# Performance work log

Measured on AMD Instinct MI355X. Metric: run time of the kernel, lower is better.

## Reference

```python
import jax, jax.numpy as jnp
import numpy as np

B, T, D, H = 2, 2048, 1024, 16
STD = 0.02

def setup_inputs() -> dict:
    key = jax.random.key(0)
    ks = jax.random.split(key, 5)
    x = jax.random.normal(ks[0], (B, T, D), dtype=jnp.float32)
    Wq = jax.random.normal(ks[1], (D, D), dtype=jnp.float32) * STD
    Wk = jax.random.normal(ks[2], (D, D), dtype=jnp.float32) * STD
    Wv = jax.random.normal(ks[3], (D, D), dtype=jnp.float32) * STD
    Wo = jax.random.normal(ks[4], (D, D), dtype=jnp.float32) * STD
    z = jnp.zeros((D,), dtype=jnp.float32)
    return {"x": x, "Wq": Wq, "bq": z, "Wk": Wk, "bk": z, "Wv": Wv, "bv": z, "Wo": Wo, "bo": z}

def _split(t, h):
    b, s, dm = t.shape
    return t.reshape(b, s, h, dm // h).transpose(0, 2, 1, 3)  # (B,h,T,d)

def reference(x, Wq, bq, Wk, bk, Wv, bv, Wo, bo):
    h = H
    # linear projections (nn.Linear: y = x @ W^T + b)
    q = _split(x @ Wq.T + bq, h)
    k = _split(x @ Wk.T + bk, h)
    v = _split(x @ Wv.T + bv, h)
    d_k = k.shape[-1]
    # scaled dot-product similarities (B,h,T,T)
    sim = jnp.einsum("bhqd,bhkd->bhqk", q, k) / jnp.sqrt(jnp.float32(d_k))
    # causal mask: upper triangle (excluding diag) filled with -inf
    Tq = sim.shape[-1]
    causal = jnp.tril(jnp.ones((Tq, Tq), dtype=bool))
    sim = jnp.where(causal, sim, -jnp.inf)
    attn = jax.nn.softmax(sim, axis=-1)
    ctx = jnp.einsum("bhqk,bhkd->bhqd", attn, v)  # (B,h,T,d)
    ctx = ctx.transpose(0, 2, 1, 3).reshape(x.shape[0], x.shape[1], -1)  # (B,T,D)
    return ctx @ Wo.T + bo
```

## Files before the change

kernel.cpp:

```cpp
#include <hip/hip_runtime.h>
#include <hip/hip_bf16.h>


typedef __attribute__((ext_vector_type(8))) short bf16x8;
typedef __attribute__((ext_vector_type(4))) float f32x4;
typedef __attribute__((ext_vector_type(4))) short s16x4;

#define QSCALE 0.18033688011f

__device__ __forceinline__ int sniff_f32(const void* p) {
    const unsigned short* u = (const unsigned short*)p;
    int c = 0;
    for (int i = 0; i < 256; ++i) {
        int e = (u[i] >> 7) & 0xFF;
        c += (e >= 0x90) ? 1 : 0;
    }
    return c > 8;
}

__device__ __forceinline__ void async_copy16(const void* g, void* l) {
    __builtin_amdgcn_global_load_lds(
        (const __attribute__((address_space(1))) void*)g,
        (__attribute__((address_space(3))) void*)l, 16, 0, 0);
}

struct Cvt { const void* src; __hip_bfloat16* dst; int n; };
struct CvtPack { Cvt a[9]; };

__global__ __launch_bounds__(256) void cvt_bf16(CvtPack pk) {
    const Cvt c = pk.a[blockIdx.y];
    const int f32 = sniff_f32(c.src);
    const int stride = gridDim.x * 256 * 8;
    for (int idx = (blockIdx.x * 256 + threadIdx.x) * 8; idx < c.n; idx += stride) {
        if (f32) {
            const float* s = (const float*)c.src + idx;
            f32x4 a0 = *(const f32x4*)s;
            f32x4 a1 = *(const f32x4*)(s + 4);
            union { __hip_bfloat16 h[8]; bf16x8 v; } u;
#pragma unroll
            for (int e = 0; e < 4; e++) u.h[e]     = (__hip_bfloat16)a0[e];
#pragma unroll
            for (int e = 0; e < 4; e++) u.h[4 + e] = (__hip_bfloat16)a1[e];
            *(bf16x8*)&c.dst[idx] = u.v;
        } else {
            *(bf16x8*)&c.dst[idx] = *(const bf16x8*)((const __hip_bfloat16*)c.src + idx);
        }
    }
}

template <int MODE>
__device__ __forceinline__ void gemm_async_body(
    const __hip_bfloat16* __restrict__ A, const __hip_bfloat16* __restrict__ W,
    const __hip_bfloat16* __restrict__ bias, void* __restrict__ C,
    int M, int N, int K, int bm, int bn, float outscale,
    __hip_bfloat16* sA, __hip_bfloat16* sB)
{
    const int tid  = threadIdx.x;
    const int wave = tid >> 6;
    const int lane = tid & 63;
    const int quad = lane >> 4;
    const int l15  = lane & 15;
    const int wr   = wave >> 1;
    const int wc   = wave & 1;

    const int srow = wave * 16 + (lane >> 2);
    const int scol = (lane & 3) * 8;
    const __hip_bfloat16* gA0 = A + (size_t)(bm + srow) * K + scol;
    const __hip_bfloat16* gB0 = W + (size_t)(bn + srow) * K + scol;
    __hip_bfloat16* sA0 = sA + wave * 512;
    __hip_bfloat16* sB0 = sB + wave * 512;

    f32x4 acc[4][4];
#pragma unroll
    for (int i = 0; i < 4; i++)
#pragma unroll
        for (int j = 0; j < 4; j++) acc[i][j] = (f32x4)0.0f;

    for (int k0 = 0; k0 < K; k0 += 32) {
        __syncthreads();
#pragma unroll
        for (int r = 0; r < 2; r++) {
            async_copy16(gA0 + (size_t)r * 64 * K + k0, sA0 + r * 2048);
            async_copy16(gB0 + (size_t)r * 64 * K + k0, sB0 + r * 2048);
        }
        __syncthreads();

        bf16x8 af[4], bf[4];
#pragma unroll
        for (int i = 0; i < 4; i++)
            af[i] = *(const bf16x8*)&sA[(wr * 64 + i * 16 + l15) * 32 + quad * 8];
#pragma unroll
        for (int j = 0; j < 4; j++)
            bf[j] = *(const bf16x8*)&sB[(wc * 64 + j * 16 + l15) * 32 + quad * 8];
#pragma unroll
        for (int i = 0; i < 4; i++)
#pragma unroll
            for (int j = 0; j < 4; j++)
                acc[i][j] = __builtin_amdgcn_mfma_f32_16x16x32_bf16(af[i], bf[j], acc[i][j], 0, 0, 0);
    }

    float bv[4];
#pragma unroll
    for (int j = 0; j < 4; j++)
        bv[j] = (float)bias[bn + wc * 64 + j * 16 + l15];

    if (MODE == 2) {
        __hip_bfloat16* sOut = sA;
        __syncthreads();
#pragma unroll
        for (int i = 0; i < 4; i++) {
            int tl = wr * 64 + i * 16 + quad * 4;
#pragma unroll
            for (int j = 0; j < 4; j++) {
                int dl = wc * 64 + j * 16 + l15;
                union { __hip_bfloat16 e[4]; s16x4 v; } u;
#pragma unroll
                for (int r = 0; r < 4; r++)
                    u.e[r] = (__hip_bfloat16)(acc[i][j][r] + bv[j]);
                *(s16x4*)&sOut[dl * 136 + tl] = u.v;
            }
        }
        __syncthreads();
        __hip_bfloat16* VTo = (__hip_bfloat16*)C;
        const int bb = bm >> 11, tt0 = bm & 2047;
#pragma unroll
        for (int g8 = 0; g8 < 8; g8++) {
            int idx = g8 * 256 + tid;
            int dl  = idx >> 4;
            int tc  = (idx & 15) * 8;
            int dg  = bn + dl;
            bf16x8 v = *(const bf16x8*)&sOut[dl * 136 + tc];
            *(bf16x8*)&VTo[(((size_t)bb * 16 + (dg >> 6)) * 64 + (dg & 63)) * 2048 + tt0 + tc] = v;
        }
    } else {
#pragma unroll
        for (int i = 0; i < 4; i++) {
#pragma unroll
            for (int j = 0; j < 4; j++) {
                int col = bn + wc * 64 + j * 16 + l15;
#pragma unroll
                for (int r = 0; r < 4; r++) {
                    int row = bm + wr * 64 + i * 16 + quad * 4 + r;
                    float v = (acc[i][j][r] + bv[j]) * outscale;
                    if (MODE == 1) ((float*)C)[(size_t)row * N + col] = v;
                    else ((__hip_bfloat16*)C)[(size_t)row * N + col] = (__hip_bfloat16)v;
                }
            }
        }
    }
}

__global__ __launch_bounds__(256, 2) void qkv_gemm(
    const __hip_bfloat16* __restrict__ x,
    const __hip_bfloat16* __restrict__ Wq, const __hip_bfloat16* __restrict__ bq, __hip_bfloat16* __restrict__ Q,
    const __hip_bfloat16* __restrict__ Wk, const __hip_bfloat16* __restrict__ bk, __hip_bfloat16* __restrict__ Kb,
    const __hip_bfloat16* __restrict__ Wv, const __hip_bfloat16* __restrict__ bv, __hip_bfloat16* __restrict__ VT,
    int M, int N, int K)
{
    __shared__ __hip_bfloat16 smem[128 * 136];
    __hip_bfloat16* sA = smem;
    __hip_bfloat16* sB = smem + 128 * 32;
    if (blockIdx.z == 0)
        gemm_async_body<0>(x, Wq, bq, Q, M, N, K, blockIdx.x * 128, blockIdx.y * 128, QSCALE, sA, sB);
    else if (blockIdx.z == 1)
        gemm_async_body<0>(x, Wk, bk, Kb, M, N, K, blockIdx.x * 128, blockIdx.y * 128, 1.0f, sA, sB);
    else
        gemm_async_body<2>(x, Wv, bv, VT, M, N, K, blockIdx.x * 128, blockIdx.y * 128, 1.0f, sA, sB);
}

template <bool OF32>
__device__ __forceinline__ void gemm64_body(
    const __hip_bfloat16* __restrict__ A, const __hip_bfloat16* __restrict__ W,
    const __hip_bfloat16* __restrict__ bias, void* __restrict__ C,
    int M, int N, int K, int bm, int bn,
    __hip_bfloat16* sA, __hip_bfloat16* sB)
{
    const int tid  = threadIdx.x;
    const int wave = tid >> 6;
    const int lane = tid & 63;
    const int quad = lane >> 4;
    const int l15  = lane & 15;

    const int srow = wave * 16 + (lane >> 2);
    const int scol = (lane & 3) * 8;
    const __hip_bfloat16* gA0 = A + (size_t)(bm + srow) * K + scol;
    const __hip_bfloat16* gB0 = W + (size_t)(bn + srow) * K + scol;
    __hip_bfloat16* sA0 = sA + wave * 512;
    __hip_bfloat16* sB0 = sB + wave * 512;

    f32x4 acc[4][2];
#pragma unroll
    for (int i = 0; i < 4; i++)
#pragma unroll
        for (int j = 0; j < 2; j++) acc[i][j] = (f32x4)0.0f;

    for (int k0 = 0; k0 < K; k0 += 32) {
        __syncthreads();
        async_copy16(gA0 + k0, sA0);
#pragma unroll
        for (int r = 0; r < 2; r++)
            async_copy16(gB0 + (size_t)r * 64 * K + k0, sB0 + r * 2048);
        __syncthreads();

        bf16x8 af[4], bf[2];
#pragma unroll
        for (int i = 0; i < 4; i++)
            af[i] = *(const bf16x8*)&sA[(i * 16 + l15) * 32 + quad * 8];
#pragma unroll
        for (int j = 0; j < 2; j++)
            bf[j] = *(const bf16x8*)&sB[(wave * 32 + j * 16 + l15) * 32 + quad * 8];
#pragma unroll
        for (int i = 0; i < 4; i++)
#pragma unroll
            for (int j = 0; j < 2; j++)
                acc[i][j] = __builtin_amdgcn_mfma_f32_16x16x32_bf16(af[i], bf[j], acc[i][j], 0, 0, 0);
    }

    float bv[2];
#pragma unroll
    for (int j = 0; j < 2; j++)
        bv[j] = (float)bias[bn + wave * 32 + j * 16 + l15];
#pragma unroll
    for (int i = 0; i < 4; i++) {
#pragma unroll
        for (int j = 0; j < 2; j++) {
            int col = bn + wave * 32 + j * 16 + l15;
#pragma unroll
            for (int r = 0; r < 4; r++) {
                int row = bm + i * 16 + quad * 4 + r;
                float v = acc[i][j][r] + bv[j];
                if (OF32) ((float*)C)[(size_t)row * N + col] = v;
                else      ((__hip_bfloat16*)C)[(size_t)row * N + col] = (__hip_bfloat16)v;
            }
        }
    }
}

__global__ __launch_bounds__(256, 2) void out_gemm(
    const __hip_bfloat16* __restrict__ A, const __hip_bfloat16* __restrict__ W,
    const __hip_bfloat16* __restrict__ bias, const void* __restrict__ origW,
    void* __restrict__ C, int M, int N, int K)
{
    __shared__ __hip_bfloat16 sA[64 * 32];
    __shared__ __hip_bfloat16 sB[128 * 32];
    __shared__ int f32flag;
    if (threadIdx.x == 0) f32flag = sniff_f32(origW);
    __syncthreads();
    if (f32flag)
        gemm64_body<true>(A, W, bias, C, M, N, K, blockIdx.x * 64, blockIdx.y * 128, sA, sB);
    else
        gemm64_body<false>(A, W, bias, C, M, N, K, blockIdx.x * 64, blockIdx.y * 128, sA, sB);
}

#define PAD 68

__global__ __launch_bounds__(512, 4) void attn_causal(
    const __hip_bfloat16* __restrict__ Q,
    const __hip_bfloat16* __restrict__ K,
    const __hip_bfloat16* __restrict__ VT,
    __hip_bfloat16* __restrict__ O,
    int T, int D, int H)
{
    __shared__ __hip_bfloat16 sK[2][64 * PAD];
    __shared__ __hip_bfloat16 sVT[2][64 * PAD];
    __shared__ __hip_bfloat16 sPA[8][16 * PAD];

    const int tid  = threadIdx.x;
    const int wave = tid >> 6;
    const int lane = tid & 63;
    const int quad = lane >> 4;
    const int l15  = lane & 15;

    const int NT = T >> 7;
    const int qt = blockIdx.z ? (NT - 1 - (int)blockIdx.x) : (int)blockIdx.x;
    const int h  = blockIdx.y;
    const int b  = blockIdx.z;
    const size_t headoff = (size_t)b * T * D + (size_t)h * 64;
    const size_t vtoff   = ((size_t)b * H + h) * 64 * (size_t)T;

    const int nkt = 2 * qt + 2;
    const int qbase    = qt * 128 + wave * 16;
    const int myrowmax = qbase + 15;

    bf16x8 qfrag[2];
#pragma unroll
    for (int kk = 0; kk < 2; kk++)
        qfrag[kk] = *(const bf16x8*)&Q[headoff +
            (size_t)(qbase + l15) * D + kk * 32 + quad * 8];

    f32x4 acc_o[4];
#pragma unroll
    for (int j = 0; j < 4; j++) acc_o[j] = (f32x4)0.0f;
    float lacc = 0.f;

    const int srow = tid >> 3;
    const int sc8  = (tid & 7) * 8;

    bf16x8 pk, pv;
    pk = *(const bf16x8*)&K[headoff + (size_t)srow * D + sc8];
    pv = *(const bf16x8*)&VT[vtoff + (size_t)srow * T + sc8];
    *(bf16x8*)&sK[0][srow * PAD + sc8]  = pk;
    *(bf16x8*)&sVT[0][srow * PAD + sc8] = pv;
    if (nkt > 1) {
        pk = *(const bf16x8*)&K[headoff + (size_t)(64 + srow) * D + sc8];
        pv = *(const bf16x8*)&VT[vtoff + (size_t)srow * T + 64 + sc8];
    }
    __syncthreads();

    for (int kt = 0; kt < nkt; ++kt) {
        const int cur = kt & 1;

        if (kt + 1 < nkt) {
            *(bf16x8*)&sK[1 - cur][srow * PAD + sc8]  = pk;
            *(bf16x8*)&sVT[1 - cur][srow * PAD + sc8] = pv;
            if (kt + 2 < nkt) {
                pk = *(const bf16x8*)&K[headoff + (size_t)((kt + 2) * 64 + srow) * D + sc8];
                pv = *(const bf16x8*)&VT[vtoff + (size_t)srow * T + (kt + 2) * 64 + sc8];
            }
        }

        if (kt * 64 <= myrowmax) {
            bf16x8 kfrag[2][4], vfrag[2][4];
#pragma unroll
            for (int kk = 0; kk < 2; kk++)
#pragma unroll
                for (int j = 0; j < 4; j++) {
                    kfrag[kk][j] = *(const bf16x8*)&sK[cur][(j * 16 + l15) * PAD + kk * 32 + quad * 8];
                    vfrag[kk][j] = *(const bf16x8*)&sVT[cur][(j * 16 + l15) * PAD + kk * 32 + quad * 8];
                }

            f32x4 st[4];
#pragma unroll
            for (int j = 0; j < 4; j++) st[j] = (f32x4)0.0f;
            __builtin_amdgcn_s_setprio(1);
#pragma unroll
            for (int kk = 0; kk < 2; kk++)
#pragma unroll
                for (int j = 0; j < 4; j++)
                    st[j] = __builtin_amdgcn_mfma_f32_16x16x32_bf16(
                        kfrag[kk][j], qfrag[kk], st[j], 0, 0, 0);
            __builtin_amdgcn_s_setprio(0);

            if (kt * 64 + 63 > qbase) {
                const int q = qbase + l15;
#pragma unroll
                for (int j = 0; j < 4; j++) {
                    int keyb = kt * 64 + j * 16 + quad * 4;
#pragma unroll
                    for (int r = 0; r < 4; r++)
                        if (keyb + r > q) st[j][r] = -1e30f;
                }
            }

#pragma unroll
            for (int j = 0; j < 4; j++) {
                union { __hip_bfloat16 e[4]; s16x4 v; } u;
#pragma unroll
                for (int r = 0; r < 4; r++) {
                    float p = exp2f(st[j][r]);
                    lacc += p;
                    u.e[r] = (__hip_bfloat16)p;
                }
                *(s16x4*)&sPA[wave][l15 * PAD + j * 16 + quad * 4] = u.v;
            }
            __builtin_amdgcn_s_setprio(1);
#pragma unroll
            for (int kk = 0; kk < 2; kk++) {
                bf16x8 a = *(const bf16x8*)&sPA[wave][l15 * PAD + kk * 32 + quad * 8];
#pragma unroll
                for (int j = 0; j < 4; j++)
                    acc_o[j] = __builtin_amdgcn_mfma_f32_16x16x32_bf16(
                        a, vfrag[kk][j], acc_o[j], 0, 0, 0);
            }
            __builtin_amdgcn_s_setprio(0);
        }

        __syncthreads();
    }

    lacc += __shfl_xor(lacc, 16, 64);
    lacc += __shfl_xor(lacc, 32, 64);

#pragma unroll
    for (int r = 0; r < 4; r++) {
        float linv = 1.0f / __shfl(lacc, quad * 4 + r, 64);
        int row = qbase + quad * 4 + r;
#pragma unroll
        for (int j = 0; j < 4; j++) {
            int col = j * 16 + l15;
            O[headoff + (size_t)row * D + col] = (__hip_bfloat16)(acc_o[j][r] * linv);
        }
    }
}

extern "C" void kernel_launch(void* const* d_in, const int* in_sizes, int n_in,
                              void* d_out, int out_size, void* d_ws, size_t ws_size,
                              hipStream_t stream) {
    const int Bb = 2, T = 2048, D = 1024, H = 16;
    const int M = Bb * T;

    __hip_bfloat16* w = (__hip_bfloat16*)d_ws;
    __hip_bfloat16* Q   = w;
    __hip_bfloat16* Kb  = Q   + (size_t)M * D;
    __hip_bfloat16* VT  = Kb  + (size_t)M * D;
    __hip_bfloat16* ctx = VT  + (size_t)M * D;
    __hip_bfloat16* xb  = ctx + (size_t)M * D;
    __hip_bfloat16* Wqb = xb  + (size_t)M * D;
    __hip_bfloat16* Wkb = Wqb + (size_t)D * D;
    __hip_bfloat16* Wvb = Wkb + (size_t)D * D;
    __hip_bfloat16* Wob = Wvb + (size_t)D * D;
    __hip_bfloat16* bqb = Wob + (size_t)D * D;
    __hip_bfloat16* bkb = bqb + D;
    __hip_bfloat16* bvb = bkb + D;
    __hip_bfloat16* bob = bvb + D;

    CvtPack pk;
    pk.a[0] = { d_in[0], xb,  M * D };
    pk.a[1] = { d_in[1], Wqb, D * D };
    pk.a[2] = { d_in[2], bqb, D };
    pk.a[3] = { d_in[3], Wkb, D * D };
    pk.a[4] = { d_in[4], bkb, D };
    pk.a[5] = { d_in[5], Wvb, D * D };
    pk.a[6] = { d_in[6], bvb, D };
    pk.a[7] = { d_in[7], Wob, D * D };
    pk.a[8] = { d_in[8], bob, D };

    cvt_bf16<<<dim3(512, 9), 256, 0, stream>>>(pk);
    qkv_gemm<<<dim3(M / 128, D / 128, 3), 256, 0, stream>>>(
        xb, Wqb, bqb, Q, Wkb, bkb, Kb, Wvb, bvb, VT, M, D, D);
    attn_causal<<<dim3(T / 128, H, Bb), 512, 0, stream>>>(Q, Kb, VT, ctx, T, D, H);
    out_gemm<<<dim3(M / 64, D / 128), 256, 0, stream>>>(
        ctx, Wob, bob, d_in[7], d_out, M, D, D);
}
```

Before: 211.1 us.

## Double-buffer LDS tiles in QKV and output GEMMs with async prefetch

Both projection GEMMs now use two LDS stages. The next K-slice is issued with global_load_lds while the current one is consumed, and the two __syncthreads per iteration become a partial vmcnt wait plus raw s_barrier. This is meant to hide global-load latency behind the MFMA work. It doubles the LDS footprint of out_gemm, and correctness depends on the hand-set vmcnt counts matching the number of outstanding loads.

Result: faster. 206.8 us (-2.0%).

```diff
diff --git a/kernel.cpp b/kernel.cpp
--- a/kernel.cpp
+++ b/kernel.cpp
@@ -53,7 +53,7 @@
     const __hip_bfloat16* __restrict__ A, const __hip_bfloat16* __restrict__ W,
     const __hip_bfloat16* __restrict__ bias, void* __restrict__ C,
     int M, int N, int K, int bm, int bn, float outscale,
-    __hip_bfloat16* sA, __hip_bfloat16* sB)
+    __hip_bfloat16* smem)
 {
     const int tid  = threadIdx.x;
     const int wave = tid >> 6;
@@ -67,8 +67,6 @@
     const int scol = (lane & 3) * 8;
     const __hip_bfloat16* gA0 = A + (size_t)(bm + srow) * K + scol;
     const __hip_bfloat16* gB0 = W + (size_t)(bn + srow) * K + scol;
-    __hip_bfloat16* sA0 = sA + wave * 512;
-    __hip_bfloat16* sB0 = sB + wave * 512;
 
     f32x4 acc[4][4];
 #pragma unroll
@@ -76,14 +74,27 @@
 #pragma unroll
         for (int j = 0; j < 4; j++) acc[i][j] = (f32x4)0.0f;
 
-    for (int k0 = 0; k0 < K; k0 += 32) {
-        __syncthreads();
-#pragma unroll
-        for (int r = 0; r < 2; r++) {
-            async_copy16(gA0 + (size_t)r * 64 * K + k0, sA0 + r * 2048);
-            async_copy16(gB0 + (size_t)r * 64 * K + k0, sB0 + r * 2048);
-        }
-        __syncthreads();
+#define QSTAGE(buf, k0) { \
+        __hip_bfloat16* d_ = smem + (buf) * 8192 + wave * 512; \
+        async_copy16(gA0 + (k0), d_); \
+        async_copy16(gA0 + (size_t)64 * K + (k0), d_ + 2048); \
+        async_copy16(gB0 + (k0), d_ + 4096); \
+        async_copy16(gB0 + (size_t)64 * K + (k0), d_ + 4096 + 2048); \
+    }
+
+    const int nt = K >> 5;
+    QSTAGE(0, 0);
+    for (int t = 0; t < nt; ++t) {
+        const int buf = t & 1;
+        const __hip_bfloat16* sA = smem + buf * 8192;
+        const __hip_bfloat16* sB = sA + 4096;
+        if (t + 1 < nt) {
+            QSTAGE(1 - buf, (t + 1) * 32);
+            asm volatile("s_waitcnt vmcnt(4)" ::: "memory");
+        } else {
+            asm volatile("s_waitcnt vmcnt(0)" ::: "memory");
+        }
+        __builtin_amdgcn_s_barrier();
 
         bf16x8 af[4], bf[4];
 #pragma unroll
@@ -97,7 +108,10 @@
 #pragma unroll
             for (int j = 0; j < 4; j++)
                 acc[i][j] = __builtin_amdgcn_mfma_f32_16x16x32_bf16(af[i], bf[j], acc[i][j], 0, 0, 0);
-    }
+
+        __builtin_amdgcn_s_barrier();
+    }
+#undef QSTAGE
 
     float bv[4];
 #pragma unroll
@@ -105,7 +119,7 @@
         bv[j] = (float)bias[bn + wc * 64 + j * 16 + l15];
 
     if (MODE == 2) {
-        __hip_bfloat16* sOut = sA;
+        __hip_bfloat16* sOut = smem;
         __syncthreads();
 #pragma unroll
         for (int i = 0; i < 4; i++) {
@@ -158,14 +172,12 @@
     int M, int N, int K)
 {
     __shared__ __hip_bfloat16 smem[128 * 136];
-    __hip_bfloat16* sA = smem;
-    __hip_bfloat16* sB = smem + 128 * 32;
     if (blockIdx.z == 0)
-        gemm_async_body<0>(x, Wq, bq, Q, M, N, K, blockIdx.x * 128, blockIdx.y * 128, QSCALE, sA, sB);
+        gemm_async_body<0>(x, Wq, bq, Q, M, N, K, blockIdx.x * 128, blockIdx.y * 128, QSCALE, smem);
     else if (blockIdx.z == 1)
-        gemm_async_body<0>(x, Wk, bk, Kb, M, N, K, blockIdx.x * 128, blockIdx.y * 128, 1.0f, sA, sB);
+        gemm_async_body<0>(x, Wk, bk, Kb, M, N, K, blockIdx.x * 128, blockIdx.y * 128, 1.0f, smem);
     else
-        gemm_async_body<2>(x, Wv, bv, VT, M, N, K, blockIdx.x * 128, blockIdx.y * 128, 1.0f, sA, sB);
+        gemm_async_body<2>(x, Wv, bv, VT, M, N, K, blockIdx.x * 128, blockIdx.y * 128, 1.0f, smem);
 }
 
 template <bool OF32>
@@ -173,7 +185,7 @@
     const __hip_bfloat16* __restrict__ A, const __hip_bfloat16* __restrict__ W,
     const __hip_bfloat16* __restrict__ bias, void* __restrict__ C,
     int M, int N, int K, int bm, int bn,
-    __hip_bfloat16* sA, __hip_bfloat16* sB)
+    __hip_bfloat16* smem)
 {
     const int tid  = threadIdx.x;
     const int wave = tid >> 6;
@@ -185,8 +197,6 @@
     const int scol = (lane & 3) * 8;
     const __hip_bfloat16* gA0 = A + (size_t)(bm + srow) * K + scol;
     const __hip_bfloat16* gB0 = W + (size_t)(bn + srow) * K + scol;
-    __hip_bfloat16* sA0 = sA + wave * 512;
-    __hip_bfloat16* sB0 = sB + wave * 512;
 
     f32x4 acc[4][2];
 #pragma unroll
@@ -194,13 +204,26 @@
 #pragma unroll
         for (int j = 0; j < 2; j++) acc[i][j] = (f32x4)0.0f;
 
-    for (int k0 = 0; k0 < K; k0 += 32) {
-        __syncthreads();
-        async_copy16(gA0 + k0, sA0);
-#pragma unroll
-        for (int r = 0; r < 2; r++)
-            async_copy16(gB0 + (size_t)r * 64 * K + k0, sB0 + r * 2048);
-        __syncthreads();
+#define OSTAGE(buf, k0) { \
+        __hip_bfloat16* d_ = smem + (buf) * 6144; \
+        async_copy16(gA0 + (k0), d_ + wave * 512); \
+        async_copy16(gB0 + (k0), d_ + 2048 + wave * 512); \
+        async_copy16(gB0 + (size_t)64 * K + (k0), d_ + 2048 + wave * 512 + 2048); \
+    }
+
+    const int nt = K >> 5;
+    OSTAGE(0, 0);
+    for (int t = 0; t < nt; ++t) {
+        const int buf = t & 1;
+        const __hip_bfloat16* sA = smem + buf * 6144;
+        const __hip_bfloat16* sB = sA + 2048;
+        if (t + 1 < nt) {
+            OSTAGE(1 - buf, (t + 1) * 32);
+            asm volatile("s_waitcnt vmcnt(3)" ::: "memory");
+        } else {
+            asm volatile("s_waitcnt vmcnt(0)" ::: "memory");
+        }
+        __builtin_amdgcn_s_barrier();
 
         bf16x8 af[4], bf[2];
 #pragma unroll
@@ -214,7 +237,10 @@
 #pragma unroll
             for (int j = 0; j < 2; j++)
                 acc[i][j] = __builtin_amdgcn_mfma_f32_16x16x32_bf16(af[i], bf[j], acc[i][j], 0, 0, 0);
-    }
+
+        __builtin_amdgcn_s_barrier();
+    }
+#undef OSTAGE
 
     float bv[2];
 #pragma unroll
@@ -241,15 +267,14 @@
     const __hip_bfloat16* __restrict__ bias, const void* __restrict__ origW,
     void* __restrict__ C, int M, int N, int K)
 {
-    __shared__ __hip_bfloat16 sA[64 * 32];
-    __shared__ __hip_bfloat16 sB[128 * 32];
+    __shared__ __hip_bfloat16 smem[2 * 6144];
     __shared__ int f32flag;
     if (threadIdx.x == 0) f32flag = sniff_f32(origW);
     __syncthreads();
     if (f32flag)
-        gemm64_body<true>(A, W, bias, C, M, N, K, blockIdx.x * 64, blockIdx.y * 128, sA, sB);
+        gemm64_body<true>(A, W, bias, C, M, N, K, blockIdx.x * 64, blockIdx.y * 128, smem);
     else
-        gemm64_body<false>(A, W, bias, C, M, N, K, blockIdx.x * 64, blockIdx.y * 128, sA, sB);
+        gemm64_body<false>(A, W, bias, C, M, N, K, blockIdx.x * 64, blockIdx.y * 128, smem);
 }
 
 #define PAD 68
```
